# Optimization experiments

Measured on AMD Instinct MI355X. Metric: run time of the kernel, lower is better.

Reference implementation:

```python
import jax, jax.numpy as jnp
import numpy as np

E = 192      # embed_dim
DI = 384     # d_inner = 2*E (mamba default expand=2)
S = 16       # d_state
R = 12       # dt_rank = ceil(E/16)
DEPTH = 4
STRIDE = 4
P = 400      # num_patches = 1600/4
NC = 20
BATCH = 32
EPS = 1e-5


def _rmsnorm(x, w):
    x = x.astype(jnp.float32)
    return x * jax.lax.rsqrt(jnp.mean(x * x, axis=-1, keepdims=True) + EPS) * w


def _mamba_mixer(h, in_w, cw, cb, xpw, dtw, dtb, a_log, d_skip, ow):
    # h: [B, L, E]
    Bsz, Ln, _ = h.shape
    xz = jnp.einsum('ble,de->bld', h, in_w)            # [B,L,2*DI]
    xm, z = xz[..., :DI], xz[..., DI:]
    # causal depthwise conv1d, kernel 4 (left pad 3, truncate to L)
    xp = jnp.pad(xm, ((0, 0), (3, 0), (0, 0)))
    xc = sum(xp[:, k:k + Ln, :] * cw[:, k] for k in range(4)) + cb
    xc = jax.nn.silu(xc)
    xdb = jnp.einsum('bld,rd->blr', xc, xpw)           # [B,L,R+2S]
    dt = jax.nn.softplus(jnp.einsum('blr,dr->bld', xdb[..., :R], dtw) + dtb)
    Bm = xdb[..., R:R + S]
    Cm = xdb[..., R + S:]
    A = -jnp.exp(a_log)                                # [DI,S]

    def step(hst, inp):
        dt_t, b_t, c_t, u_t = inp                      # [B,DI],[B,S],[B,S],[B,DI]
        dA = jnp.exp(dt_t[:, :, None] * A)             # [B,DI,S]
        hst = dA * hst + (dt_t * u_t)[:, :, None] * b_t[:, None, :]
        y_t = jnp.einsum('bdn,bn->bd', hst, c_t)
        return hst, y_t

    h0 = jnp.zeros((Bsz, DI, S), xc.dtype)
    xs = (dt.transpose(1, 0, 2), Bm.transpose(1, 0, 2), Cm.transpose(1, 0, 2), xc.transpose(1, 0, 2))
    _, ys = jax.lax.scan(step, h0, xs)
    y = ys.transpose(1, 0, 2) + xc * d_skip
    y = y * jax.nn.silu(z)
    return jnp.einsum('bld,ed->ble', y, ow)


def _forward(imgs, patch_w, patch_b, cls_token, pos_embed, cnn_w, cnn_b, norm_w,
             in_proj_w, conv_w, conv_b, x_proj_w, dt_proj_w, dt_proj_b, A_log, D,
             out_proj_w, norm_f_w, head_w, head_b):
    Bsz = imgs.shape[0]
    # StrideEmbed: conv1d kernel=stride=4 == reshape + matmul
    x = imgs.reshape(Bsz, P, STRIDE)
    x = jnp.einsum('blk,ek->ble', x, patch_w[:, 0, :]) + patch_b   # [B,P,E]
    x = x + pos_embed[:, :-1, :]
    # depthwise conv1d k=3 pad=1 over length
    xp = jnp.pad(x, ((0, 0), (1, 1), (0, 0)))
    x = sum(xp[:, k:k + P, :] * cnn_w[:, 0, k] for k in range(3)) + cnn_b
    cls = cls_token + pos_embed[:, -1, :]                           # [1,1,E]
    x = jnp.concatenate([x, jnp.broadcast_to(cls, (Bsz, 1, E))], axis=1)  # [B,401,E]

    hidden = x
    residual = None
    for i in range(DEPTH):
        residual = hidden if residual is None else residual + hidden
        hn = _rmsnorm(residual, norm_w[i])
        hidden = _mamba_mixer(hn, in_proj_w[i], conv_w[i], conv_b[i], x_proj_w[i],
                              dt_proj_w[i], dt_proj_b[i], A_log[i], D[i], out_proj_w[i])
    out = _rmsnorm(hidden + residual, norm_f_w)
    v_sem = out[:, -1, :]
    return v_sem @ head_w.T + head_b


def setup_inputs() -> dict:
    key = jax.random.key(0)
    ks = jax.random.split(key, 12)
    n = lambda k, shp, s=0.02: jax.random.normal(k, shp, dtype=jnp.float32) * s
    return {
        'imgs': jax.random.normal(ks[0], (BATCH, 1, 40, 40), jnp.float32),
        'patch_w': n(ks[1], (E, 1, STRIDE), 0.3),
        'patch_b': jnp.zeros((E,), jnp.float32),
        'cls_token': n(ks[2], (1, 1, E)),
        'pos_embed': n(ks[3], (1, P + 1, E)),
        'cnn_w': n(ks[4], (E, 1, 3), 0.3),
        'cnn_b': jnp.zeros((E,), jnp.float32),
        'norm_w': jnp.ones((DEPTH, E), jnp.float32),
        'in_proj_w': n(ks[5], (DEPTH, 2 * DI, E), 0.05),
        'conv_w': n(ks[6], (DEPTH, DI, 4), 0.3),
        'conv_b': jnp.zeros((DEPTH, DI), jnp.float32),
        'x_proj_w': n(ks[7], (DEPTH, R + 2 * S, DI), 0.05),
        'dt_proj_w': n(ks[8], (DEPTH, DI, R), 0.3),
        'dt_proj_b': jnp.log(jnp.expm1(jax.random.uniform(ks[9], (DEPTH, DI), minval=0.001, maxval=0.1))),
        'A_log': jnp.log(jnp.broadcast_to(jnp.arange(1, S + 1, dtype=jnp.float32), (DEPTH, DI, S))),
        'D': jnp.ones((DEPTH, DI), jnp.float32),
        'out_proj_w': n(ks[10], (DEPTH, E, DI), 0.05),
        'norm_f_w': jnp.ones((E,), jnp.float32),
        'head_w': n(ks[11], (NC, E)),
        'head_b': jnp.zeros((NC,), jnp.float32),
    }


def reference(imgs, patch_w, patch_b, cls_token, pos_embed, cnn_w, cnn_b, norm_w,
              in_proj_w, conv_w, conv_b, x_proj_w, dt_proj_w, dt_proj_b, A_log, D,
              out_proj_w, norm_f_w, head_w, head_b):
    return _forward(imgs, patch_w, patch_b, cls_token, pos_embed, cnn_w, cnn_b, norm_w,
                    in_proj_w, conv_w, conv_b, x_proj_w, dt_proj_w, dt_proj_b, A_log, D,
                    out_proj_w, norm_f_w, head_w, head_b)
```

## Files before the change

kernel.cpp:

```cpp
#include <hip/hip_runtime.h>
#include <math.h>

#define E 192
#define DI 384
#define S 16
#define R 12
#define DEPTH 4
#define P 400
#define NC 20
#define BATCH 32
#define L 401
#define NTOK (BATCH * L)
#define CH 32
#define NCH 13

using short8 = __attribute__((ext_vector_type(8))) short;
using float4v = __attribute__((ext_vector_type(4))) float;

__device__ __forceinline__ float siluf(float x) {
    return x / (1.f + __expf(-x));
}
__device__ __forceinline__ float softplusf(float x) {
    return (x > 20.f) ? x : log1pf(__expf(x));
}
__device__ __forceinline__ unsigned short f2bf(float x) {
    unsigned int u = __float_as_uint(x);
    unsigned int r = 0x7fffu + ((u >> 16) & 1u);
    return (unsigned short)((u + r) >> 16);
}

__global__ void k_embed(const float* __restrict__ imgs, const float* __restrict__ patch_w,
                        const float* __restrict__ patch_b, const float* __restrict__ cls_token,
                        const float* __restrict__ pos_embed, const float* __restrict__ cnn_w,
                        const float* __restrict__ cnn_b, float* __restrict__ resid) {
    int idx = blockIdx.x * blockDim.x + threadIdx.x;
    if (idx >= NTOK * E) return;
    int e = idx % E;
    int bl = idx / E;
    int l = bl % L;
    int b = bl / L;
    float out;
    if (l == P) {
        out = cls_token[e] + pos_embed[(size_t)P * E + e];
    } else {
        float w0 = patch_w[e * 4 + 0], w1 = patch_w[e * 4 + 1];
        float w2 = patch_w[e * 4 + 2], w3 = patch_w[e * 4 + 3];
        float pb = patch_b[e];
        const float* ib = imgs + (size_t)b * 1600;
        auto xe = [&](int ll) -> float {
            const float* ip = ib + ll * 4;
            return ip[0] * w0 + ip[1] * w1 + ip[2] * w2 + ip[3] * w3 + pb +
                   pos_embed[(size_t)ll * E + e];
        };
        float c0 = cnn_w[e * 3 + 0], c1 = cnn_w[e * 3 + 1], c2 = cnn_w[e * 3 + 2];
        float acc = cnn_b[e] + xe(l) * c1;
        if (l > 0) acc += xe(l - 1) * c0;
        if (l < P - 1) acc += xe(l + 1) * c2;
        out = acc;
    }
    resid[idx] = out;
}

template <bool ADD>
__global__ void k_rmsnorm(const float* __restrict__ hidden, float* __restrict__ resid,
                          unsigned short* __restrict__ hn, const float* __restrict__ w) {
    int wave = blockIdx.x * (blockDim.x >> 6) + (threadIdx.x >> 6);
    int lane = threadIdx.x & 63;
    if (wave >= NTOK) return;
    size_t base = (size_t)wave * E;
    float v[3];
    float ss = 0.f;
#pragma unroll
    for (int j = 0; j < 3; j++) {
        int e = lane + j * 64;
        float r = resid[base + e];
        if (ADD) {
            r += hidden[base + e];
            resid[base + e] = r;
        }
        v[j] = r;
        ss += r * r;
    }
#pragma unroll
    for (int off = 32; off > 0; off >>= 1) ss += __shfl_xor(ss, off, 64);
    float scale = rsqrtf(ss * (1.f / (float)E) + 1e-5f);
#pragma unroll
    for (int j = 0; j < 3; j++) {
        int e = lane + j * 64;
        hn[base + e] = f2bf(v[j] * scale * w[e]);
    }
}

__global__ void k_prep(const float* __restrict__ in_proj_w, const float* __restrict__ x_proj_w,
                       const float* __restrict__ out_proj_w, const float* __restrict__ A_log,
                       const float* __restrict__ dt_proj_w,
                       unsigned short* __restrict__ w_in, unsigned short* __restrict__ w_x,
                       unsigned short* __restrict__ w_out, float* __restrict__ negA,
                       float* __restrict__ dtw_t) {
    const int n1 = DEPTH * 2 * DI * E;
    const int n2 = DEPTH * 44 * DI;
    const int n3 = DEPTH * E * DI;
    const int n4 = DEPTH * DI * S;
    const int n5 = DEPTH * DI * R;
    int idx = blockIdx.x * blockDim.x + threadIdx.x;
    if (idx < n1) {
        w_in[idx] = f2bf(in_proj_w[idx]);
    } else if (idx < n1 + n2) {
        int i = idx - n1;
        w_x[i] = f2bf(x_proj_w[i]);
    } else if (idx < n1 + n2 + n3) {
        int i = idx - n1 - n2;
        w_out[i] = f2bf(out_proj_w[i]);
    } else if (idx < n1 + n2 + n3 + n4) {
        int i = idx - n1 - n2 - n3;
        int layer = i / (DI * S);
        int rem = i % (DI * S);
        int n = rem / DI;
        int d = rem % DI;
        negA[i] = -__expf(A_log[(size_t)layer * DI * S + d * S + n]);
    } else if (idx < n1 + n2 + n3 + n4 + n5) {
        int i = idx - n1 - n2 - n3 - n4;
        int layer = i / (DI * R);
        int rem = i % (DI * R);
        int r = rem / DI;
        int d = rem % DI;
        dtw_t[i] = dt_proj_w[(size_t)layer * DI * R + d * R + r];
    }
}

__global__ void k_flag(const float* __restrict__ negA, int* __restrict__ flag) {
    int idx = blockIdx.x * blockDim.x + threadIdx.x;
    if (idx >= DEPTH * DI) return;
    int layer = idx / DI;
    int d = idx % DI;
    const float* base = negA + (size_t)layer * DI * S;
    float a0 = base[d];
    bool ok = true;
#pragma unroll
    for (int n = 1; n < S; n++) {
        float an = base[n * DI + d];
        ok = ok && (fabsf(an - (float)(n + 1) * a0) <= 1e-5f * fabsf(an));
    }
    flag[idx] = ok ? 1 : 0;
}

template <int BM, int BN>
__global__ __launch_bounds__(256) void k_gemm_bf16(const unsigned short* __restrict__ A,
                                                   const unsigned short* __restrict__ W,
                                                   float* __restrict__ C, int M, int N, int K) {
    constexpr int BK = 64, PADK = BK + 8;
    constexpr int MT = BM / 32, NT = BN / 32;
    __shared__ unsigned short As[BM][PADK];
    __shared__ unsigned short Bs[BN][PADK];
    int tid = threadIdx.x;
    int m0 = blockIdx.y * BM, n0 = blockIdx.x * BN;
    int wave = tid >> 6, lane = tid & 63;
    int row16 = lane & 15, quad = lane >> 4;
    int wm0 = (wave >> 1) * (BM / 2), wn0 = (wave & 1) * (BN / 2);

    float4v acc[MT][NT];
#pragma unroll
    for (int i = 0; i < MT; i++)
#pragma unroll
        for (int j = 0; j < NT; j++) acc[i][j] = (float4v){0.f, 0.f, 0.f, 0.f};

    for (int k0 = 0; k0 < K; k0 += BK) {
#pragma unroll
        for (int p = 0; p < MT; p++) {
            int idx = (p * 256 + tid) * 8;
            int row = idx / BK, col = idx % BK;
            int gm = m0 + row;
            short8 v;
            if (gm < M)
                v = *(const short8*)&A[(size_t)gm * K + k0 + col];
            else
                v = (short8)0;
            *(short8*)&As[row][col] = v;
        }
#pragma unroll
        for (int p = 0; p < NT; p++) {
            int idx = (p * 256 + tid) * 8;
            int row = idx / BK, col = idx % BK;
            int gn = n0 + row;
            short8 v;
            if (gn < N)
                v = *(const short8*)&W[(size_t)gn * K + k0 + col];
            else
                v = (short8)0;
            *(short8*)&Bs[row][col] = v;
        }
        __syncthreads();
#pragma unroll
        for (int kk = 0; kk < BK; kk += 32) {
            int koff = kk + quad * 8;
            short8 af[MT], bfr[NT];
#pragma unroll
            for (int i = 0; i < MT; i++)
                af[i] = *(const short8*)&As[wm0 + i * 16 + row16][koff];
#pragma unroll
            for (int j = 0; j < NT; j++)
                bfr[j] = *(const short8*)&Bs[wn0 + j * 16 + row16][koff];
#pragma unroll
            for (int i = 0; i < MT; i++)
#pragma unroll
                for (int j = 0; j < NT; j++)
                    acc[i][j] = __builtin_amdgcn_mfma_f32_16x16x32_bf16(af[i], bfr[j],
                                                                        acc[i][j], 0, 0, 0);
        }
        __syncthreads();
    }
#pragma unroll
    for (int i = 0; i < MT; i++) {
#pragma unroll
        for (int j = 0; j < NT; j++) {
#pragma unroll
            for (int r = 0; r < 4; r++) {
                int m = m0 + wm0 + i * 16 + quad * 4 + r;
                int n = n0 + wn0 + j * 16 + row16;
                if (m < M && n < N) C[(size_t)m * N + n] = acc[i][j][r];
            }
        }
    }
}

__global__ void k_conv(const float* __restrict__ xz, const float* __restrict__ cw,
                       const float* __restrict__ cb, float* __restrict__ xc,
                       unsigned short* __restrict__ xc_bf) {
    int idx = blockIdx.x * blockDim.x + threadIdx.x;
    if (idx >= NTOK * DI) return;
    int d = idx % DI;
    int bl = idx / DI;
    int l = bl % L;
    int b = bl / L;
    const float* base = xz + (size_t)b * L * (2 * DI) + d;
    float acc = cb[d];
#pragma unroll
    for (int k = 0; k < 4; k++) {
        int ll = l - 3 + k;
        if (ll >= 0) acc += base[(size_t)ll * (2 * DI)] * cw[d * 4 + k];
    }
    float v = siluf(acc);
    xc[idx] = v;
    xc_bf[idx] = f2bf(v);
}

__global__ __launch_bounds__(384) void k_dtpre(
        const float* __restrict__ xdb, const float* __restrict__ dtw_t,
        const float* __restrict__ dtb, const float* __restrict__ negA_l,
        float2* __restrict__ dte1) {
    int tok = blockIdx.x;
    int d = threadIdx.x;
    const float* xr = xdb + (size_t)tok * 44;
    float acc = dtb[d];
#pragma unroll
    for (int r = 0; r < R; r++) acc += xr[r] * dtw_t[r * DI + d];
    float dtv = softplusf(acc);
    float e1 = __expf(negA_l[d] * dtv);
    dte1[(size_t)tok * DI + d] = make_float2(dtv, e1);
}

__global__ __launch_bounds__(384) void k_scanA(
        const float* __restrict__ xc, const float* __restrict__ xdb,
        const float2* __restrict__ dte1, const float* __restrict__ negA_l,
        const int* __restrict__ flag_l, const float* __restrict__ Dskip,
        float* __restrict__ ylocal, float* __restrict__ dtcum,
        float* __restrict__ hend) {
    int d = threadIdx.x;
    int ch = blockIdx.x;
    int b = blockIdx.y;
    int t0 = ch * CH;
    int t1 = min(t0 + CH, L);
    bool fast = __all(flag_l[d] != 0);
    float a[S];
    if (!fast) {
#pragma unroll
        for (int n = 0; n < S; n++) a[n] = negA_l[n * DI + d];
    }
    float dsk = Dskip[d];
    float h[S] = {};
    float dts = 0.f;
    size_t tok0 = (size_t)b * L + t0;
    float2 de = dte1[tok0 * DI + d];
    float u = xc[tok0 * DI + d];
    for (int t = t0; t < t1; t++) {
        size_t tok = (size_t)b * L + t;
        float dtv = de.x, e1v = de.y, uu = u;
        if (t + 1 < t1) {
            de = dte1[(tok + 1) * DI + d];
            u = xc[(tok + 1) * DI + d];
        }
        const float* row = xdb + tok * 44;
        dts += dtv;
        float dtu = dtv * uu;
        float y = uu * dsk;
        if (fast) {
            float p = e1v;
#pragma unroll
            for (int n = 0; n < S; n++) {
                h[n] = p * h[n] + dtu * row[R + n];
                y += h[n] * row[R + S + n];
                p *= e1v;
            }
        } else {
#pragma unroll
            for (int n = 0; n < S; n++) {
                float dA = __expf(dtv * a[n]);
                h[n] = dA * h[n] + dtu * row[R + n];
                y += h[n] * row[R + S + n];
            }
        }
        ylocal[tok * DI + d] = y;
        dtcum[tok * DI + d] = dts;
    }
    float* he = hend + ((size_t)(b * NCH + ch) * S) * DI + d;
#pragma unroll
    for (int n = 0; n < S; n++) he[n * DI] = h[n];
}

__global__ void k_scanB(const float* __restrict__ hend, const float* __restrict__ dtcum,
                        const float* __restrict__ negA_l, const int* __restrict__ flag_l,
                        float* __restrict__ hinit) {
    int idx = blockIdx.x * blockDim.x + threadIdx.x;
    if (idx >= BATCH * DI) return;
    int d = idx % DI;
    int b = idx / DI;
    bool fast = __all(flag_l[d] != 0);
    float a[S];
#pragma unroll
    for (int n = 0; n < S; n++) a[n] = negA_l[n * DI + d];
    float h[S] = {};
    for (int ch = 0; ch < NCH; ch++) {
        size_t o = ((size_t)(b * NCH + ch) * S) * DI + d;
#pragma unroll
        for (int n = 0; n < S; n++) hinit[o + n * DI] = h[n];
        int tlast = min(ch * CH + CH, L) - 1;
        float dts = dtcum[((size_t)b * L + tlast) * DI + d];
        if (fast) {
            float e1c = __expf(a[0] * dts);
            float p = e1c;
#pragma unroll
            for (int n = 0; n < S; n++) {
                h[n] = p * h[n] + hend[o + n * DI];
                p *= e1c;
            }
        } else {
#pragma unroll
            for (int n = 0; n < S; n++) h[n] = __expf(dts * a[n]) * h[n] + hend[o + n * DI];
        }
    }
}

__global__ __launch_bounds__(384) void k_fixup(
        const float* __restrict__ xz, const float* __restrict__ xdb,
        const float* __restrict__ negA_l, const int* __restrict__ flag_l,
        const float* __restrict__ hinit, const float* __restrict__ ylocal,
        const float* __restrict__ dtcum, unsigned short* __restrict__ y_bf) {
    int tok = blockIdx.x;
    int d = threadIdx.x;
    int l = tok % L;
    int b = tok / L;
    int ch = l / CH;
    size_t idx = (size_t)tok * DI + d;
    float y = ylocal[idx];
    if (ch != 0) {
        bool fast = __all(flag_l[d] != 0);
        const float* h0 = hinit + ((size_t)(b * NCH + ch) * S) * DI + d;
        const float* cv = xdb + (size_t)tok * 44 + R + S;
        float dts = dtcum[idx];
        float corr = 0.f;
        if (fast) {
            float e1c = __expf(negA_l[d] * dts);
            float p = e1c;
#pragma unroll
            for (int n = 0; n < S; n++) {
                corr += cv[n] * p * h0[n * DI];
                p *= e1c;
            }
        } else {
#pragma unroll
            for (int n = 0; n < S; n++)
                corr += cv[n] * __expf(negA_l[n * DI + d] * dts) * h0[n * DI];
        }
        y += corr;
    }
    float z = xz[(size_t)tok * (2 * DI) + DI + d];
    y_bf[idx] = f2bf(y * siluf(z));
}

__global__ void k_head(const float* __restrict__ resid, const float* __restrict__ hidden,
                       const float* __restrict__ norm_f_w, const float* __restrict__ head_w,
                       const float* __restrict__ head_b, float* __restrict__ out) {
    __shared__ float v[E];
    int b = blockIdx.x;
    int lane = threadIdx.x;
    size_t base = ((size_t)b * L + P) * E;
    float loc[3];
    float ss = 0.f;
#pragma unroll
    for (int j = 0; j < 3; j++) {
        int e = lane + j * 64;
        float x = resid[base + e] + hidden[base + e];
        loc[j] = x;
        ss += x * x;
    }
#pragma unroll
    for (int off = 32; off > 0; off >>= 1) ss += __shfl_xor(ss, off, 64);
    float scale = rsqrtf(ss * (1.f / (float)E) + 1e-5f);
#pragma unroll
    for (int j = 0; j < 3; j++) {
        int e = lane + j * 64;
        v[e] = loc[j] * scale * norm_f_w[e];
    }
    __syncthreads();
    if (lane < NC) {
        float acc = head_b[lane];
        for (int e = 0; e < E; e++) acc += v[e] * head_w[lane * E + e];
        out[b * NC + lane] = acc;
    }
}

extern "C" void kernel_launch(void* const* d_in, const int* in_sizes, int n_in,
                              void* d_out, int out_size, void* d_ws, size_t ws_size,
                              hipStream_t stream) {
    const float* imgs      = (const float*)d_in[0];
    const float* patch_w   = (const float*)d_in[1];
    const float* patch_b   = (const float*)d_in[2];
    const float* cls_token = (const float*)d_in[3];
    const float* pos_embed = (const float*)d_in[4];
    const float* cnn_w     = (const float*)d_in[5];
    const float* cnn_b     = (const float*)d_in[6];
    const float* norm_w    = (const float*)d_in[7];
    const float* in_proj_w = (const float*)d_in[8];
    const float* conv_w    = (const float*)d_in[9];
    const float* conv_b    = (const float*)d_in[10];
    const float* x_proj_w  = (const float*)d_in[11];
    const float* dt_proj_w = (const float*)d_in[12];
    const float* dt_proj_b = (const float*)d_in[13];
    const float* A_log     = (const float*)d_in[14];
    const float* Dskip     = (const float*)d_in[15];
    const float* out_proj_w= (const float*)d_in[16];
    const float* norm_f_w  = (const float*)d_in[17];
    const float* head_w    = (const float*)d_in[18];
    const float* head_b    = (const float*)d_in[19];

    float* ws = (float*)d_ws;
    size_t off = 0;
    float* resid  = ws + off; off += (size_t)NTOK * E;
    float* hidden = ws + off; off += (size_t)NTOK * E;
    float* xz     = ws + off; off += (size_t)NTOK * 2 * DI;
    float* xc     = ws + off; off += (size_t)NTOK * DI;
    float* xdb    = ws + off; off += (size_t)NTOK * 44;
    float* dte1   = ws + off; off += (size_t)NTOK * DI * 2;
    float* ylocal = ws + off; off += (size_t)NTOK * DI;
    float* dtcum  = ws + off; off += (size_t)NTOK * DI;
    float* hend   = ws + off; off += (size_t)BATCH * NCH * DI * S;
    float* hinit  = ws + off; off += (size_t)BATCH * NCH * DI * S;
    float* negA   = ws + off; off += (size_t)DEPTH * DI * S;
    float* dtw_t  = ws + off; off += (size_t)DEPTH * DI * R;
    int*   gflag  = (int*)(ws + off); off += (size_t)DEPTH * DI;
    unsigned short* bf_buf = (unsigned short*)(ws + off); off += (size_t)NTOK * DI / 2;
    unsigned short* w_in  = (unsigned short*)(ws + off); off += (size_t)DEPTH * 2 * DI * E / 2;
    unsigned short* w_x   = (unsigned short*)(ws + off); off += (size_t)DEPTH * 44 * DI / 2 + 16;
    unsigned short* w_out = (unsigned short*)(ws + off); off += (size_t)DEPTH * E * DI / 2;

    unsigned short* hn_bf = bf_buf;
    unsigned short* xc_bf = bf_buf;
    unsigned short* y_bf  = bf_buf;

    {
        int ntot = DEPTH * (2 * DI * E + 44 * DI + E * DI + DI * S + DI * R);
        k_prep<<<(ntot + 255) / 256, 256, 0, stream>>>(in_proj_w, x_proj_w, out_proj_w, A_log,
                                                       dt_proj_w, w_in, w_x, w_out, negA,
                                                       dtw_t);
        k_flag<<<(DEPTH * DI + 255) / 256, 256, 0, stream>>>(negA, gflag);
    }

    k_embed<<<(NTOK * E) / 256, 256, 0, stream>>>(imgs, patch_w, patch_b, cls_token,
                                                  pos_embed, cnn_w, cnn_b, resid);

    for (int i = 0; i < DEPTH; i++) {
        if (i == 0)
            k_rmsnorm<false><<<NTOK / 4, 256, 0, stream>>>(hidden, resid, hn_bf, norm_w + i * E);
        else
            k_rmsnorm<true><<<NTOK / 4, 256, 0, stream>>>(hidden, resid, hn_bf, norm_w + i * E);

        {
            dim3 g((2 * DI) / 64, (NTOK + 127) / 128);
            k_gemm_bf16<128, 64><<<g, 256, 0, stream>>>(hn_bf, w_in + (size_t)i * 2 * DI * E,
                                                        xz, NTOK, 2 * DI, E);
        }
        k_conv<<<(NTOK * DI) / 256, 256, 0, stream>>>(xz, conv_w + (size_t)i * DI * 4,
                                                      conv_b + (size_t)i * DI, xc, xc_bf);
        {
            dim3 g(1, NTOK / 32);
            k_gemm_bf16<32, 64><<<g, 256, 0, stream>>>(xc_bf, w_x + (size_t)i * 44 * DI, xdb,
                                                       NTOK, 44, DI);
        }
        const float* nA = negA + (size_t)i * DI * S;
        const int* fl = gflag + (size_t)i * DI;
        k_dtpre<<<NTOK, 384, 0, stream>>>(xdb, dtw_t + (size_t)i * DI * R,
                                          dt_proj_b + (size_t)i * DI, nA, (float2*)dte1);
        {
            dim3 g(NCH, BATCH);
            k_scanA<<<g, DI, 0, stream>>>(xc, xdb, (const float2*)dte1, nA, fl,
                                          Dskip + (size_t)i * DI, ylocal, dtcum, hend);
            k_scanB<<<(BATCH * DI + 255) / 256, 256, 0, stream>>>(hend, dtcum, nA, fl, hinit);
            k_fixup<<<NTOK, 384, 0, stream>>>(xz, xdb, nA, fl, hinit, ylocal, dtcum, y_bf);
        }
        {
            dim3 g(E / 64, (NTOK + 63) / 64);
            k_gemm_bf16<64, 64><<<g, 256, 0, stream>>>(y_bf, w_out + (size_t)i * E * DI,
                                                       hidden, NTOK, E, DI);
        }
    }

    k_head<<<BATCH, 64, 0, stream>>>(resid, hidden, norm_f_w, head_w, head_b, (float*)d_out);
}
```

Before: 772.7 us.

## Fuse dt projection into x_proj GEMM, split xz output, halve scan chunk

The dt_proj/softplus/exp precompute is folded into the x_proj GEMM epilogue, with the xdb tile staged in shared memory, which removes a separate kernel launch and one re-read of xdb. The in_proj GEMM now uses 128x128 tiles and writes the x half as fp32 and the z gate as bf16 into separate buffers, cutting the bytes that conv and fixup read. The scan chunk length drops from 32 to 16, doubling the number of chunks so more blocks can run in parallel. The cost is more chunk-boundary fixup work and a bf16-rounded z gate.

```diff
diff --git a/kernel.cpp b/kernel.cpp
--- a/kernel.cpp
+++ b/kernel.cpp
@@ -11,8 +11,8 @@
 #define BATCH 32
 #define L 401
 #define NTOK (BATCH * L)
-#define CH 32
-#define NCH 13
+#define CH 16
+#define NCH 26
 
 using short8 = __attribute__((ext_vector_type(8))) short;
 using float4v = __attribute__((ext_vector_type(4))) float;
@@ -27,6 +27,9 @@
     unsigned int u = __float_as_uint(x);
     unsigned int r = 0x7fffu + ((u >> 16) & 1u);
     return (unsigned short)((u + r) >> 16);
+}
+__device__ __forceinline__ float bf2f(unsigned short v) {
+    return __uint_as_float(((unsigned int)v) << 16);
 }
 
 __global__ void k_embed(const float* __restrict__ imgs, const float* __restrict__ patch_w,
@@ -144,10 +147,12 @@
     flag[idx] = ok ? 1 : 0;
 }
 
-template <int BM, int BN>
+template <int BM, int BN, int EPI>
 __global__ __launch_bounds__(256) void k_gemm_bf16(const unsigned short* __restrict__ A,
                                                    const unsigned short* __restrict__ W,
-                                                   float* __restrict__ C, int M, int N, int K) {
+                                                   float* __restrict__ C,
+                                                   unsigned short* __restrict__ Z,
+                                                   int M, int N, int K) {
     constexpr int BK = 64, PADK = BK + 8;
     constexpr int MT = BM / 32, NT = BN / 32;
     __shared__ unsigned short As[BM][PADK];
@@ -217,13 +222,97 @@
             for (int r = 0; r < 4; r++) {
                 int m = m0 + wm0 + i * 16 + quad * 4 + r;
                 int n = n0 + wn0 + j * 16 + row16;
-                if (m < M && n < N) C[(size_t)m * N + n] = acc[i][j][r];
+                if (m >= M || n >= N) continue;
+                float v = acc[i][j][r];
+                if (EPI == 0) {
+                    C[(size_t)m * N + n] = v;
+                } else {
+                    if (n < DI)
+                        C[(size_t)m * DI + n] = v;
+                    else
+                        Z[(size_t)m * DI + (n - DI)] = f2bf(v);
+                }
             }
         }
     }
 }
 
-__global__ void k_conv(const float* __restrict__ xz, const float* __restrict__ cw,
+__global__ __launch_bounds__(256) void k_gemm_xproj(
+        const unsigned short* __restrict__ A, const unsigned short* __restrict__ W,
+        const float* __restrict__ dtw_t, const float* __restrict__ dtb,
+        const float* __restrict__ negA_l, float* __restrict__ xdb,
+        float2* __restrict__ dte1) {
+    constexpr int BM = 32, BN = 64, BK = 64, PADK = BK + 8;
+    const int N = 44, K = DI;
+    __shared__ unsigned short As[BM][PADK];
+    __shared__ unsigned short Bs[BN][PADK];
+    __shared__ float Cs[BM][N + 4];
+    int tid = threadIdx.x;
+    int m0 = blockIdx.x * BM;
+    int wave = tid >> 6, lane = tid & 63;
+    int row16 = lane & 15, quad = lane >> 4;
+    int wm0 = (wave >> 1) * 16, wn0 = (wave & 1) * 32;
+
+    float4v acc[2];
+    acc[0] = (float4v){0.f, 0.f, 0.f, 0.f};
+    acc[1] = (float4v){0.f, 0.f, 0.f, 0.f};
+
+    for (int k0 = 0; k0 < K; k0 += BK) {
+        {
+            int idx = tid * 8;
+            int row = idx / BK, col = idx % BK;
+            *(short8*)&As[row][col] = *(const short8*)&A[(size_t)(m0 + row) * K + k0 + col];
+        }
+#pragma unroll
+        for (int p = 0; p < 2; p++) {
+            int idx = (p * 256 + tid) * 8;
+            int row = idx / BK, col = idx % BK;
+            short8 v;
+            if (row < N)
+                v = *(const short8*)&W[(size_t)row * K + k0 + col];
+            else
+                v = (short8)0;
+            *(short8*)&Bs[row][col] = v;
+        }
+        __syncthreads();
+#pragma unroll
+        for (int kk = 0; kk < BK; kk += 32) {
+            int koff = kk + quad * 8;
+            short8 af = *(const short8*)&As[wm0 + row16][koff];
+#pragma unroll
+            for (int j = 0; j < 2; j++) {
+                short8 bfr = *(const short8*)&Bs[wn0 + j * 16 + row16][koff];
+                acc[j] = __builtin_amdgcn_mfma_f32_16x16x32_bf16(af, bfr, acc[j], 0, 0, 0);
+            }
+        }
+        __syncthreads();
+    }
+#pragma unroll
+    for (int j = 0; j < 2; j++) {
+#pragma unroll
+        for (int r = 0; r < 4; r++) {
+            int row = wm0 + quad * 4 + r;
+            int n = wn0 + j * 16 + row16;
+            if (n < N) Cs[row][n] = acc[j][r];
+        }
+    }
+    __syncthreads();
+    for (int idx = tid; idx < BM * N; idx += 256) {
+        int row = idx / N, n = idx % N;
+        xdb[(size_t)(m0 + row) * N + n] = Cs[row][n];
+    }
+    for (int idx = tid; idx < BM * DI; idx += 256) {
+        int row = idx / DI, d = idx % DI;
+        float acc2 = dtb[d];
+#pragma unroll
+        for (int r = 0; r < R; r++) acc2 += Cs[row][r] * dtw_t[r * DI + d];
+        float dtv = softplusf(acc2);
+        float e1 = __expf(negA_l[d] * dtv);
+        dte1[(size_t)(m0 + row) * DI + d] = make_float2(dtv, e1);
+    }
+}
+
+__global__ void k_conv(const float* __restrict__ xm, const float* __restrict__ cw,
                        const float* __restrict__ cb, float* __restrict__ xc,
                        unsigned short* __restrict__ xc_bf) {
     int idx = blockIdx.x * blockDim.x + threadIdx.x;
@@ -232,31 +321,16 @@
     int bl = idx / DI;
     int l = bl % L;
     int b = bl / L;
-    const float* base = xz + (size_t)b * L * (2 * DI) + d;
+    const float* base = xm + (size_t)b * L * DI + d;
     float acc = cb[d];
 #pragma unroll
     for (int k = 0; k < 4; k++) {
         int ll = l - 3 + k;
-        if (ll >= 0) acc += base[(size_t)ll * (2 * DI)] * cw[d * 4 + k];
+        if (ll >= 0) acc += base[(size_t)ll * DI] * cw[d * 4 + k];
     }
     float v = siluf(acc);
     xc[idx] = v;
     xc_bf[idx] = f2bf(v);
-}
-
-__global__ __launch_bounds__(384) void k_dtpre(
-        const float* __restrict__ xdb, const float* __restrict__ dtw_t,
-        const float* __restrict__ dtb, const float* __restrict__ negA_l,
-        float2* __restrict__ dte1) {
-    int tok = blockIdx.x;
-    int d = threadIdx.x;
-    const float* xr = xdb + (size_t)tok * 44;
-    float acc = dtb[d];
-#pragma unroll
-    for (int r = 0; r < R; r++) acc += xr[r] * dtw_t[r * DI + d];
-    float dtv = softplusf(acc);
-    float e1 = __expf(negA_l[d] * dtv);
-    dte1[(size_t)tok * DI + d] = make_float2(dtv, e1);
 }
 
 __global__ __launch_bounds__(384) void k_scanA(
@@ -351,7 +425,7 @@
 }
 
 __global__ __launch_bounds__(384) void k_fixup(
-        const float* __restrict__ xz, const float* __restrict__ xdb,
+        const unsigned short* __restrict__ z_bf, const float* __restrict__ xdb,
         const float* __restrict__ negA_l, const int* __restrict__ flag_l,
         const float* __restrict__ hinit, const float* __restrict__ ylocal,
         const float* __restrict__ dtcum, unsigned short* __restrict__ y_bf) {
@@ -383,7 +457,7 @@
         }
         y += corr;
     }
-    float z = xz[(size_t)tok * (2 * DI) + DI + d];
+    float z = bf2f(z_bf[idx]);
     y_bf[idx] = f2bf(y * siluf(z));
 }
 
@@ -447,7 +521,7 @@
     size_t off = 0;
     float* resid  = ws + off; off += (size_t)NTOK * E;
     float* hidden = ws + off; off += (size_t)NTOK * E;
-    float* xz     = ws + off; off += (size_t)NTOK * 2 * DI;
+    float* xm     = ws + off; off += (size_t)NTOK * DI;
     float* xc     = ws + off; off += (size_t)NTOK * DI;
     float* xdb    = ws + off; off += (size_t)NTOK * 44;
     float* dte1   = ws + off; off += (size_t)NTOK * DI * 2;
@@ -458,6 +532,7 @@
     float* negA   = ws + off; off += (size_t)DEPTH * DI * S;
     float* dtw_t  = ws + off; off += (size_t)DEPTH * DI * R;
     int*   gflag  = (int*)(ws + off); off += (size_t)DEPTH * DI;
+    unsigned short* z_bf   = (unsigned short*)(ws + off); off += (size_t)NTOK * DI / 2;
     unsigned short* bf_buf = (unsigned short*)(ws + off); off += (size_t)NTOK * DI / 2;
     unsigned short* w_in  = (unsigned short*)(ws + off); off += (size_t)DEPTH * 2 * DI * E / 2;
     unsigned short* w_x   = (unsigned short*)(ws + off); off += (size_t)DEPTH * 44 * DI / 2 + 16;
@@ -485,32 +560,28 @@
             k_rmsnorm<true><<<NTOK / 4, 256, 0, stream>>>(hidden, resid, hn_bf, norm_w + i * E);
 
         {
-            dim3 g((2 * DI) / 64, (NTOK + 127) / 128);
-            k_gemm_bf16<128, 64><<<g, 256, 0, stream>>>(hn_bf, w_in + (size_t)i * 2 * DI * E,
-                                                        xz, NTOK, 2 * DI, E);
-        }
-        k_conv<<<(NTOK * DI) / 256, 256, 0, stream>>>(xz, conv_w + (size_t)i * DI * 4,
+            dim3 g((2 * DI) / 128, (NTOK + 127) / 128);
+            k_gemm_bf16<128, 128, 1><<<g, 256, 0, stream>>>(
+                hn_bf, w_in + (size_t)i * 2 * DI * E, xm, z_bf, NTOK, 2 * DI, E);
+        }
+        k_conv<<<(NTOK * DI) / 256, 256, 0, stream>>>(xm, conv_w + (size_t)i * DI * 4,
                                                       conv_b + (size_t)i * DI, xc, xc_bf);
-        {
-            dim3 g(1, NTOK / 32);
-            k_gemm_bf16<32, 64><<<g, 256, 0, stream>>>(xc_bf, w_x + (size_t)i * 44 * DI, xdb,
-                                                       NTOK, 44, DI);
-        }
         const float* nA = negA + (size_t)i * DI * S;
         const int* fl = gflag + (size_t)i * DI;
-        k_dtpre<<<NTOK, 384, 0, stream>>>(xdb, dtw_t + (size_t)i * DI * R,
-                                          dt_proj_b + (size_t)i * DI, nA, (float2*)dte1);
+        k_gemm_xproj<<<NTOK / 32, 256, 0, stream>>>(
+            xc_bf, w_x + (size_t)i * 44 * DI, dtw_t + (size_t)i * DI * R,
+            dt_proj_b + (size_t)i * DI, nA, xdb, (float2*)dte1);
         {
             dim3 g(NCH, BATCH);
             k_scanA<<<g, DI, 0, stream>>>(xc, xdb, (const float2*)dte1, nA, fl,
                                           Dskip + (size_t)i * DI, ylocal, dtcum, hend);
             k_scanB<<<(BATCH * DI + 255) / 256, 256, 0, stream>>>(hend, dtcum, nA, fl, hinit);
-            k_fixup<<<NTOK, 384, 0, stream>>>(xz, xdb, nA, fl, hinit, ylocal, dtcum, y_bf);
+            k_fixup<<<NTOK, 384, 0, stream>>>(z_bf, xdb, nA, fl, hinit, ylocal, dtcum, y_bf);
         }
         {
             dim3 g(E / 64, (NTOK + 63) / 64);
-            k_gemm_bf16<64, 64><<<g, 256, 0, stream>>>(y_bf, w_out + (size_t)i * E * DI,
-                                                       hidden, NTOK, E, DI);
+            k_gemm_bf16<64, 64, 0><<<g, 256, 0, stream>>>(
+                y_bf, w_out + (size_t)i * E * DI, hidden, nullptr, NTOK, E, DI);
         }
     }
 
```

After: 862.5 us. 1.12x slower.
